# Kernel optimization log

Hardware: AMD Instinct MI355X
Metric: run time of the kernel (lower is better)

The kernel has to match this reference:

```python
import jax, jax.numpy as jnp
import numpy as np

# --- dims (match init_kwargs) ---
B, T, S, K = 4, 128, 64, 2
CS = 1024            # codebook_size
NOTE_V, PHON_V = 128, 64
NE, PE, SE, PGB, PGE = 128, 128, 16, 8, 32
COND, TOK, PREV, D = 256, 256, 256, 512
NH, L_CTX, L_AUD = 8, 4, 6
HIST_WIN, AUD_WIN = 32, 64
DFF = 4 * D

CTX_KEYS = ["ln1_w","ln1_b","in_w","in_b","out_w","out_b","ln2_w","ln2_b","f1_w","f1_b","f2_w","f2_b"]


def _ln(x, w, b):
    m = x.mean(-1, keepdims=True)
    v = ((x - m) ** 2).mean(-1, keepdims=True)
    return (x - m) / jnp.sqrt(v + 1e-5) * w + b


def _mlp2(x, w1, b1, w2, b2, act):
    return act(x @ w1.T + b1) @ w2.T + b2


def _local_mask(n, win):
    i = jnp.arange(n)
    d = i[:, None] - i[None, :]
    return (d < 0) | (d >= win)   # True = masked (causal, local window)


def _mha(x, mask, in_w, in_b, out_w, out_b, nh):
    b, s, d = x.shape
    dh = d // nh
    q, k, v = jnp.split(x @ in_w.T + in_b, 3, axis=-1)
    sp = lambda t: t.reshape(b, s, nh, dh).transpose(0, 2, 1, 3)
    q, k, v = sp(q), sp(k), sp(v)
    sc = jnp.einsum('bhqd,bhkd->bhqk', q, k) * (1.0 / np.sqrt(dh))
    sc = jnp.where(mask, -1e9, sc)
    a = jax.nn.softmax(sc, axis=-1)
    o = jnp.einsum('bhqk,bhkd->bhqd', a, v).transpose(0, 2, 1, 3).reshape(b, s, d)
    return o @ out_w.T + out_b


def _block(x, mask, pr, nh):
    # pr: dict with ln1_w..f2_b for one layer (pre-norm attn + FFN, GELU)
    h = _ln(x, pr["ln1_w"], pr["ln1_b"])
    x = x + _mha(h, mask, pr["in_w"], pr["in_b"], pr["out_w"], pr["out_b"], nh)
    h2 = _ln(x, pr["ln2_w"], pr["ln2_b"])
    return x + _mlp2(h2, pr["f1_w"], pr["f1_b"], pr["f2_w"], pr["f2_b"],
                     lambda z: jax.nn.gelu(z, approximate=False))


def _forward(p, codes, note_id, phoneme_id, slur, phone_progress):
    silu = jax.nn.silu
    # ---- condition encoder ----
    cond_in = jnp.concatenate([
        p["note_emb_w"][note_id], p["phoneme_emb_w"][phoneme_id],
        p["slur_emb_w"][jnp.clip(slur, 0, 1)], p["pp_emb_w"][phone_progress]], -1)
    cond = _mlp2(cond_in, p["cond_w1"], p["cond_b1"], p["cond_w2"], p["cond_b2"], silu)
    # ---- shifted prev-step representation ----
    first = codes[..., 0]                       # [B,T,S]
    pooled = p["token_emb_w"][first].mean(2)    # [B,T,TOK]
    prev = _mlp2(pooled, p["prev_w1"], p["prev_b1"], p["prev_w2"], p["prev_b2"], silu)
    bos = jnp.broadcast_to(p["bos_step"], (B, 1, PREV))
    prev = jnp.concatenate([bos, prev[:, :-1]], 1)
    # ---- context transformer over steps (local causal window) ----
    h = _mlp2(jnp.concatenate([cond, prev], -1), p["step_w1"], p["step_b1"], p["step_w2"], p["step_b2"], silu)
    m_ctx = _local_mask(T, HIST_WIN)
    for l in range(L_CTX):
        pr = {k: p["ctx_" + k][l] for k in CTX_KEYS}
        h = _block(h, m_ctx, pr, NH)
    # ---- audio decoder over frames within each step ----
    tok = p["token_emb_w"][first] @ p["audio_in_w"].T + p["audio_in_b"]   # [B,T,S,D]
    bos_a = jnp.broadcast_to(p["audio_bos"], (B, T, 1, D))
    a = jnp.concatenate([bos_a, tok[:, :, :-1]], 2) + p["frame_pos"][None, None] + h[:, :, None]
    a = a.reshape(B * T, S, D)
    m_a = _local_mask(S, min(AUD_WIN, S))
    for l in range(L_AUD):
        pr = {k: p["aud_" + k][l] for k in CTX_KEYS}
        a = _block(a, m_a, pr, NH)
    ah = a.reshape(B, T, S, D)
    # ---- heads ----
    first_logits = (ah @ p["first_w"].T + p["first_b"])[..., None, :]     # [B,T,S,1,CS]
    rh = _mlp2(jnp.concatenate([ah, tok], -1), p["resc_w1"], p["resc_b1"], p["resc_w2"], p["resc_b2"], silu)
    res = jnp.einsum('btsd,kcd->btskc', rh, p["res_w"]) + p["res_b"]       # [B,T,S,K-1,CS]
    return jnp.concatenate([first_logits, res], axis=3)                    # [B,T,S,K,CS]


def setup_inputs() -> dict:
    key = jax.random.key(0)
    ks = iter(jax.random.split(key, 128))
    w = lambda *sh: jax.random.normal(next(ks), sh, jnp.float32) * 0.02
    z = lambda *sh: jnp.zeros(sh, jnp.float32)
    o = lambda *sh: jnp.ones(sh, jnp.float32)
    inp = {
        "codes": jax.random.randint(next(ks), (B, T, S, K), 0, CS, jnp.int32),
        "note_id": jax.random.randint(next(ks), (B, T), 0, NOTE_V, jnp.int32),
        "phoneme_id": jax.random.randint(next(ks), (B, T), 0, PHON_V, jnp.int32),
        "slur": jax.random.randint(next(ks), (B, T), 0, 2, jnp.int32),
        "phone_progress": jax.random.randint(next(ks), (B, T), 0, PGB, jnp.int32),
        "note_emb_w": w(NOTE_V, NE), "phoneme_emb_w": w(PHON_V, PE),
        "slur_emb_w": w(2, SE), "pp_emb_w": w(PGB, PGE),
        "cond_w1": w(COND, NE + PE + SE + PGE), "cond_b1": z(COND),
        "cond_w2": w(COND, COND), "cond_b2": z(COND),
        "token_emb_w": w(CS, TOK),
        "prev_w1": w(PREV, TOK), "prev_b1": z(PREV),
        "prev_w2": w(PREV, PREV), "prev_b2": z(PREV),
        "bos_step": z(PREV),
        "step_w1": w(D, COND + PREV), "step_b1": z(D),
        "step_w2": w(D, D), "step_b2": z(D),
        "audio_in_w": w(D, TOK), "audio_in_b": z(D),
        "audio_bos": z(D), "frame_pos": w(S, D),
        "first_w": w(CS, D), "first_b": z(CS),
        "resc_w1": w(D, 2 * D), "resc_b1": z(D),
        "resc_w2": w(D, D), "resc_b2": z(D),
        "res_w": w(K - 1, CS, D), "res_b": z(K - 1, CS),
    }
    for pre, L in (("ctx_", L_CTX), ("aud_", L_AUD)):
        inp[pre + "ln1_w"] = o(L, D); inp[pre + "ln1_b"] = z(L, D)
        inp[pre + "in_w"] = w(L, 3 * D, D); inp[pre + "in_b"] = z(L, 3 * D)
        inp[pre + "out_w"] = w(L, D, D); inp[pre + "out_b"] = z(L, D)
        inp[pre + "ln2_w"] = o(L, D); inp[pre + "ln2_b"] = z(L, D)
        inp[pre + "f1_w"] = w(L, DFF, D); inp[pre + "f1_b"] = z(L, DFF)
        inp[pre + "f2_w"] = w(L, D, DFF); inp[pre + "f2_b"] = z(L, D)
    return inp


FLOAT_KEYS = ["note_emb_w","phoneme_emb_w","slur_emb_w","pp_emb_w","cond_w1","cond_b1","cond_w2","cond_b2","token_emb_w","prev_w1","prev_b1","prev_w2","prev_b2","bos_step","step_w1","step_b1","step_w2","step_b2","audio_in_w","audio_in_b","audio_bos","frame_pos","first_w","first_b","resc_w1","resc_b1","resc_w2","resc_b2","res_w","res_b"] + [p + k for p in ("ctx_","aud_") for k in CTX_KEYS]


def reference(codes, note_id, phoneme_id, slur, phone_progress,
              note_emb_w, phoneme_emb_w, slur_emb_w, pp_emb_w,
              cond_w1, cond_b1, cond_w2, cond_b2, token_emb_w,
              prev_w1, prev_b1, prev_w2, prev_b2, bos_step,
              step_w1, step_b1, step_w2, step_b2,
              audio_in_w, audio_in_b, audio_bos, frame_pos,
              first_w, first_b, resc_w1, resc_b1, resc_w2, resc_b2, res_w, res_b,
              ctx_ln1_w, ctx_ln1_b, ctx_in_w, ctx_in_b, ctx_out_w, ctx_out_b,
              ctx_ln2_w, ctx_ln2_b, ctx_f1_w, ctx_f1_b, ctx_f2_w, ctx_f2_b,
              aud_ln1_w, aud_ln1_b, aud_in_w, aud_in_b, aud_out_w, aud_out_b,
              aud_ln2_w, aud_ln2_b, aud_f1_w, aud_f1_b, aud_f2_w, aud_f2_b):
    loc = locals()
    p = {k: loc[k] for k in FLOAT_KEYS}
    return _forward(p, codes, note_id, phoneme_id, slur, phone_progress)
```

## Files before the change

kernel.cpp:

```cpp
#include <hip/hip_runtime.h>
#include <cstdint>
#include <cstddef>

typedef unsigned short u16;
typedef short bf16x8 __attribute__((ext_vector_type(8)));
typedef float f32x4 __attribute__((ext_vector_type(4)));

__device__ __forceinline__ float bf2f(u16 u) { return __uint_as_float(((unsigned)u) << 16); }
__device__ __forceinline__ u16 f2bf(float f) {
  unsigned i = __float_as_uint(f);
  i += 0x7fffu + ((i >> 16) & 1u);
  return (u16)(i >> 16);
}
__device__ __forceinline__ unsigned packbf2(float lo, float hi) {
  return (unsigned)f2bf(lo) | ((unsigned)f2bf(hi) << 16);
}
__device__ __forceinline__ float lo16(unsigned u) { return __uint_as_float(u << 16); }
__device__ __forceinline__ float hi16(unsigned u) { return __uint_as_float(u & 0xffff0000u); }

__device__ __forceinline__ void async_ld16(u16* lds, const u16* g) {
  __builtin_amdgcn_global_load_lds((const __attribute__((address_space(1))) void*)g,
                                   (__attribute__((address_space(3))) void*)lds, 16, 0, 0);
}

__global__ void k_cast8(const float4* __restrict__ x, uint4* __restrict__ y, int n8) {
  int i = blockIdx.x * 256 + threadIdx.x;
  if (i >= n8) return;
  float4 a = x[(size_t)i * 2], b = x[(size_t)i * 2 + 1];
  uint4 o;
  o.x = packbf2(a.x, a.y); o.y = packbf2(a.z, a.w);
  o.z = packbf2(b.x, b.y); o.w = packbf2(b.z, b.w);
  y[i] = o;
}

template<int ACT, int OUTM>
__global__ __launch_bounds__(256)
void gemm_mfma(const u16* __restrict__ A, const u16* __restrict__ W,
               const float* __restrict__ bias, void* __restrict__ Cp,
               int M, int N, int K, int ldc) {
  __shared__ u16 As[3][128 * 32];
  __shared__ u16 Bs[3][128 * 32];
  const int tid = threadIdx.x;
  const int wave = tid >> 6, lane = tid & 63;

  const int gx = gridDim.x;
  const int nwg = gx * (int)gridDim.y;
  const int flat = (int)blockIdx.y * gx + (int)blockIdx.x;
  const int xcd = flat & 7, lo = flat >> 3;
  const int q = nwg >> 3, r = nwg & 7;
  const int swz = (xcd < r ? xcd * (q + 1) : r * (q + 1) + (xcd - r) * q) + lo;
  const int bm = (swz / gx) * 128, bn = (swz % gx) * 128;

  const int wm = (wave & 1) * 64, wn = (wave >> 1) * 64;
  const int srow = tid >> 2, selem = (tid & 3) * 8;
  const u16* Ap0 = A + (size_t)(bm + srow) * K + selem;
  const u16* Ap1 = A + (size_t)(bm + srow + 64) * K + selem;
  const u16* Wp0 = W + (size_t)(bn + srow) * K + selem;
  const u16* Wp1 = W + (size_t)(bn + srow + 64) * K + selem;
  const int fr = lane & 15, fq = (lane >> 4) * 8;

  f32x4 acc[4][4];
#pragma unroll
  for (int i = 0; i < 4; ++i)
#pragma unroll
    for (int j = 0; j < 4; ++j) acc[i][j] = (f32x4){0.f, 0.f, 0.f, 0.f};

  const int nt = K >> 5;

  auto stage = [&](int buf, int k0) {
    u16* AsD = &As[buf][tid * 8];
    u16* BsD = &Bs[buf][tid * 8];
    async_ld16(AsD, Ap0 + k0);
    async_ld16(AsD + 2048, Ap1 + k0);
    async_ld16(BsD, Wp0 + k0);
    async_ld16(BsD + 2048, Wp1 + k0);
  };

  stage(0, 0);
  if (nt > 1) stage(1, 32);

  int bi = 0;
  for (int t = 0; t < nt; ++t) {
    if (t + 1 < nt) asm volatile("s_waitcnt vmcnt(4)" ::: "memory");
    else            asm volatile("s_waitcnt vmcnt(0)" ::: "memory");
    __builtin_amdgcn_s_barrier();
    if (t + 2 < nt) {
      int nb = bi + 2; if (nb >= 3) nb -= 3;
      stage(nb, (t + 2) << 5);
    }
    const u16* Asb = As[bi];
    const u16* Bsb = Bs[bi];
    bf16x8 af[4], bfv[4];
#pragma unroll
    for (int i = 0; i < 4; ++i)
      af[i] = *(const bf16x8*)&Asb[(wm + i * 16 + fr) * 32 + fq];
#pragma unroll
    for (int j = 0; j < 4; ++j)
      bfv[j] = *(const bf16x8*)&Bsb[(wn + j * 16 + fr) * 32 + fq];
#pragma unroll
    for (int i = 0; i < 4; ++i)
#pragma unroll
      for (int j = 0; j < 4; ++j)
        acc[i][j] = __builtin_amdgcn_mfma_f32_16x16x32_bf16(af[i], bfv[j], acc[i][j], 0, 0, 0);
    if (++bi == 3) bi = 0;
  }

  const int mr = bm + wm + (lane >> 4) * 4;
  const int nc = bn + wn + (lane & 15);
#pragma unroll
  for (int j = 0; j < 4; ++j) {
    int n = nc + j * 16;
    float bv = bias[n];
#pragma unroll
    for (int i = 0; i < 4; ++i) {
      int mbase = mr + i * 16;
#pragma unroll
      for (int r = 0; r < 4; ++r) {
        float v = acc[i][j][r] + bv;
        if (ACT == 1) v = v / (1.f + __expf(-v));
        else if (ACT == 2) v = 0.5f * v * (1.f + erff(v * 0.70710678118f));
        size_t off = (size_t)(mbase + r) * ldc + n;
        if (OUTM == 0) ((u16*)Cp)[off] = f2bf(v);
        else if (OUTM == 1) ((float*)Cp)[off] += v;
        else ((float*)Cp)[off] = v;
      }
    }
  }
}

__global__ __launch_bounds__(256)
void k_layernorm(const float* __restrict__ X, const float* __restrict__ w,
                 const float* __restrict__ b, u16* __restrict__ Y) {
  int row = blockIdx.x, tid = threadIdx.x;
  const float* x = X + (size_t)row * 512;
  float v0 = x[tid], v1 = x[tid + 256];
  __shared__ float red[4];
  float s = v0 + v1;
  for (int o = 32; o; o >>= 1) s += __shfl_down(s, o, 64);
  if ((tid & 63) == 0) red[tid >> 6] = s;
  __syncthreads();
  if (tid == 0) red[0] = (red[0] + red[1] + red[2] + red[3]) * (1.f / 512.f);
  __syncthreads();
  float mean = red[0];
  __syncthreads();
  float d0 = v0 - mean, d1 = v1 - mean;
  float q = d0 * d0 + d1 * d1;
  for (int o = 32; o; o >>= 1) q += __shfl_down(q, o, 64);
  if ((tid & 63) == 0) red[tid >> 6] = q;
  __syncthreads();
  if (tid == 0) red[0] = (red[0] + red[1] + red[2] + red[3]) * (1.f / 512.f);
  __syncthreads();
  float rstd = rsqrtf(red[0] + 1e-5f);
  size_t o0 = (size_t)row * 512 + tid;
  Y[o0] = f2bf(d0 * rstd * w[tid] + b[tid]);
  Y[o0 + 256] = f2bf(d1 * rstd * w[tid + 256] + b[tid + 256]);
}

__global__ void k_cond_gather(const int* __restrict__ note_id, const int* __restrict__ phon_id,
                              const int* __restrict__ slur, const int* __restrict__ pp,
                              const float* __restrict__ note_emb, const float* __restrict__ phon_emb,
                              const float* __restrict__ slur_emb, const float* __restrict__ pp_emb,
                              u16* __restrict__ out) {
  int bt = blockIdx.x, t = threadIdx.x;
  u16 v = 0;
  if (t < 128) v = f2bf(note_emb[note_id[bt] * 128 + t]);
  else if (t < 256) v = f2bf(phon_emb[phon_id[bt] * 128 + (t - 128)]);
  else if (t < 272) {
    int sv = slur[bt]; sv = sv < 0 ? 0 : (sv > 1 ? 1 : sv);
    v = f2bf(slur_emb[sv * 16 + (t - 256)]);
  } else if (t < 304) v = f2bf(pp_emb[pp[bt] * 32 + (t - 272)]);
  out[bt * 320 + t] = v;
}

__global__ void k_pad_w(const float* __restrict__ w, u16* __restrict__ out) {
  int n = blockIdx.x, t = threadIdx.x;
  out[n * 320 + t] = (t < 304) ? f2bf(w[n * 304 + t]) : (u16)0;
}

__global__ void k_femb(const int* __restrict__ codes, const uint4* __restrict__ emb,
                       uint4* __restrict__ out) {
  int i = blockIdx.x * 256 + threadIdx.x;
  int m = i >> 5, c = i & 31;
  out[i] = emb[(size_t)codes[m * 2] * 32 + c];
}

__global__ void k_pool(const u16* __restrict__ femb, u16* __restrict__ pooled) {
  int bt = blockIdx.x, c = threadIdx.x;
  float s = 0.f;
  for (int j = 0; j < 64; ++j) s += bf2f(femb[((size_t)bt * 64 + j) * 256 + c]);
  pooled[bt * 256 + c] = f2bf(s * (1.f / 64.f));
}

__global__ void k_stepin(const u16* __restrict__ cond, const u16* __restrict__ prevo,
                         const float* __restrict__ bosf, u16* __restrict__ out) {
  int bt = blockIdx.x, t = threadIdx.x;
  u16 v;
  if (t < 256) v = cond[bt * 256 + t];
  else {
    int tt = bt & 127;
    v = (tt == 0) ? f2bf(bosf[t - 256]) : prevo[(bt - 1) * 256 + (t - 256)];
  }
  out[bt * 512 + t] = v;
}

__global__ __launch_bounds__(64)
void k_ctx_attn(const u16* __restrict__ qkv, u16* __restrict__ out) {
  int t = blockIdx.x, h = blockIdx.y, b = blockIdx.z;
  int lane = threadIdx.x;
  int bt = b * 128 + t;
  float qd = bf2f(qkv[(size_t)bt * 1536 + h * 64 + lane]) * 0.125f;
  int klo = t - 31; if (klo < 0) klo = 0;
  int n = t - klo + 1;
  __shared__ float sc[32];
  for (int i = 0; i < n; ++i) {
    float p = qd * bf2f(qkv[((size_t)(b * 128 + klo + i)) * 1536 + 512 + h * 64 + lane]);
    for (int o = 32; o; o >>= 1) p += __shfl_xor(p, o, 64);
    if (lane == 0) sc[i] = p;
  }
  __syncthreads();
  float mx = -1e30f;
  for (int i = 0; i < n; ++i) mx = fmaxf(mx, sc[i]);
  float den = 0.f, acc = 0.f;
  for (int i = 0; i < n; ++i) {
    float p = __expf(sc[i] - mx);
    den += p;
    acc += p * bf2f(qkv[((size_t)(b * 128 + klo + i)) * 1536 + 1024 + h * 64 + lane]);
  }
  out[(size_t)bt * 512 + h * 64 + lane] = f2bf(acc / den);
}

__global__ __launch_bounds__(128)
void k_aud_attn_mfma(const u16* __restrict__ qkv, u16* __restrict__ out) {
  constexpr int LP = 66;
  __shared__ u16 Pl[2][64 * LP];
  __shared__ u16 Vt[2][64 * LP];
  const int wave = threadIdx.x >> 6, lane = threadIdx.x & 63;
  const int id = blockIdx.x * 2 + wave;
  const int seq = id >> 3, h = id & 7;
  const u16* Qb = qkv + (size_t)seq * 64 * 1536 + h * 64;
  const u16* Kb = Qb + 512;
  const u16* Vb = Qb + 1024;
  u16* Plw = Pl[wave];
  u16* Vtw = Vt[wave];
  const int fr = lane & 15, fq = (lane >> 4) * 8;

#pragma unroll
  for (int t = 0; t < 8; ++t) {
    int vr = (lane >> 3) + 8 * t, vc = (lane & 7) * 8;
    uint4 vv = *(const uint4*)(Vb + (size_t)vr * 1536 + vc);
    Vtw[(vc + 0) * LP + vr] = (u16)(vv.x & 0xffff);
    Vtw[(vc + 1) * LP + vr] = (u16)(vv.x >> 16);
    Vtw[(vc + 2) * LP + vr] = (u16)(vv.y & 0xffff);
    Vtw[(vc + 3) * LP + vr] = (u16)(vv.y >> 16);
    Vtw[(vc + 4) * LP + vr] = (u16)(vv.z & 0xffff);
    Vtw[(vc + 5) * LP + vr] = (u16)(vv.z >> 16);
    Vtw[(vc + 6) * LP + vr] = (u16)(vv.w & 0xffff);
    Vtw[(vc + 7) * LP + vr] = (u16)(vv.w >> 16);
  }

  bf16x8 aq[4][2], bk[4][2];
#pragma unroll
  for (int i = 0; i < 4; ++i)
#pragma unroll
    for (int c = 0; c < 2; ++c) {
      aq[i][c] = *(const bf16x8*)(Qb + (size_t)(i * 16 + fr) * 1536 + fq + 32 * c);
      bk[i][c] = *(const bf16x8*)(Kb + (size_t)(i * 16 + fr) * 1536 + fq + 32 * c);
    }
  f32x4 s[4][4];
#pragma unroll
  for (int i = 0; i < 4; ++i)
#pragma unroll
    for (int j = 0; j < 4; ++j) s[i][j] = (f32x4){0.f, 0.f, 0.f, 0.f};
#pragma unroll
  for (int c = 0; c < 2; ++c)
#pragma unroll
    for (int i = 0; i < 4; ++i)
#pragma unroll
      for (int j = 0; j < 4; ++j)
        s[i][j] = __builtin_amdgcn_mfma_f32_16x16x32_bf16(aq[i][c], bk[j][c], s[i][j], 0, 0, 0);

  const int qr = (lane >> 4) * 4;
#pragma unroll
  for (int i = 0; i < 4; ++i) {
#pragma unroll
    for (int r = 0; r < 4; ++r) {
      int row = 16 * i + qr + r;
      float mx = -1e30f;
      float vj[4];
#pragma unroll
      for (int j = 0; j < 4; ++j) {
        float v = s[i][j][r] * 0.125f;
        if (16 * j + fr > row) v = -1e30f;
        vj[j] = v;
        mx = fmaxf(mx, v);
      }
      for (int o = 8; o; o >>= 1) mx = fmaxf(mx, __shfl_xor(mx, o, 64));
      float den = 0.f;
#pragma unroll
      for (int j = 0; j < 4; ++j) { vj[j] = __expf(vj[j] - mx); den += vj[j]; }
      for (int o = 8; o; o >>= 1) den += __shfl_xor(den, o, 64);
      float inv = 1.f / den;
#pragma unroll
      for (int j = 0; j < 4; ++j)
        Plw[row * LP + 16 * j + fr] = f2bf(vj[j] * inv);
    }
  }
  __syncthreads();

  f32x4 o4[4][4];
#pragma unroll
  for (int i = 0; i < 4; ++i)
#pragma unroll
    for (int j = 0; j < 4; ++j) o4[i][j] = (f32x4){0.f, 0.f, 0.f, 0.f};
#pragma unroll
  for (int c = 0; c < 2; ++c) {
    bf16x8 ap[4], bv[4];
#pragma unroll
    for (int i = 0; i < 4; ++i)
      ap[i] = *(const bf16x8*)&Plw[(16 * i + fr) * LP + fq + 32 * c];
#pragma unroll
    for (int j = 0; j < 4; ++j)
      bv[j] = *(const bf16x8*)&Vtw[(16 * j + fr) * LP + fq + 32 * c];
#pragma unroll
    for (int i = 0; i < 4; ++i)
#pragma unroll
      for (int j = 0; j < 4; ++j)
        o4[i][j] = __builtin_amdgcn_mfma_f32_16x16x32_bf16(ap[i], bv[j], o4[i][j], 0, 0, 0);
  }
#pragma unroll
  for (int i = 0; i < 4; ++i)
#pragma unroll
    for (int r = 0; r < 4; ++r) {
      int row = 16 * i + qr + r;
      u16* ob = out + ((size_t)seq * 64 + row) * 512 + h * 64;
#pragma unroll
      for (int j = 0; j < 4; ++j) ob[16 * j + fr] = f2bf(o4[i][j][r]);
    }
}

__global__ void k_abuild(const uint4* __restrict__ tok, const float4* __restrict__ bosf,
                         const float4* __restrict__ fpos, const float4* __restrict__ hstep,
                         float4* __restrict__ a) {
  size_t i = (size_t)blockIdx.x * 256 + threadIdx.x;
  int d8 = (int)(i & 63);
  size_t row = i >> 6;
  int s = (int)(row & 63);
  size_t bt = row >> 6;
  float t0, t1, t2, t3, t4, t5, t6, t7;
  if (s == 0) {
    float4 b0 = bosf[d8 * 2], b1 = bosf[d8 * 2 + 1];
    t0 = b0.x; t1 = b0.y; t2 = b0.z; t3 = b0.w;
    t4 = b1.x; t5 = b1.y; t6 = b1.z; t7 = b1.w;
  } else {
    uint4 tv = tok[(row - 1) * 64 + d8];
    t0 = lo16(tv.x); t1 = hi16(tv.x); t2 = lo16(tv.y); t3 = hi16(tv.y);
    t4 = lo16(tv.z); t5 = hi16(tv.z); t6 = lo16(tv.w); t7 = hi16(tv.w);
  }
  float4 f0 = fpos[(size_t)s * 128 + d8 * 2], f1 = fpos[(size_t)s * 128 + d8 * 2 + 1];
  float4 h0 = hstep[bt * 128 + d8 * 2], h1 = hstep[bt * 128 + d8 * 2 + 1];
  float4 o0, o1;
  o0.x = t0 + f0.x + h0.x; o0.y = t1 + f0.y + h0.y;
  o0.z = t2 + f0.z + h0.z; o0.w = t3 + f0.w + h0.w;
  o1.x = t4 + f1.x + h1.x; o1.y = t5 + f1.y + h1.y;
  o1.z = t6 + f1.z + h1.z; o1.w = t7 + f1.w + h1.w;
  a[i * 2] = o0; a[i * 2 + 1] = o1;
}

__global__ void k_cat(const uint4* __restrict__ ah, const uint4* __restrict__ tok,
                      uint4* __restrict__ out) {
  size_t i = (size_t)blockIdx.x * 256 + threadIdx.x;
  size_t m = i >> 7;
  int c = (int)(i & 127);
  out[i] = (c < 64) ? ah[m * 64 + c] : tok[m * 64 + (c - 64)];
}

template<int ACT, int OUTM>
static inline void gemm(const u16* A, const u16* W, const float* bias, void* C,
                        int M, int N, int K, int ldc, hipStream_t s) {
  gemm_mfma<ACT, OUTM><<<dim3(N / 128, M / 128), 256, 0, s>>>(A, W, bias, C, M, N, K, ldc);
}

static inline void cast_bf16(const float* x, u16* y, size_t n, hipStream_t s) {
  int n8 = (int)(n / 8);
  k_cast8<<<(n8 + 255) / 256, 256, 0, s>>>((const float4*)x, (uint4*)y, n8);
}

extern "C" void kernel_launch(void* const* d_in, const int* in_sizes, int n_in,
                              void* d_out, int out_size, void* d_ws, size_t ws_size,
                              hipStream_t stream) {
  const int* codes    = (const int*)d_in[0];
  const int* note_id  = (const int*)d_in[1];
  const int* phon_id  = (const int*)d_in[2];
  const int* slur     = (const int*)d_in[3];
  const int* pprog    = (const int*)d_in[4];
  const float* note_emb = (const float*)d_in[5];
  const float* phon_emb = (const float*)d_in[6];
  const float* slur_emb = (const float*)d_in[7];
  const float* pp_emb   = (const float*)d_in[8];
  const float* cond_w1  = (const float*)d_in[9];
  const float* cond_b1  = (const float*)d_in[10];
  const float* cond_w2  = (const float*)d_in[11];
  const float* cond_b2  = (const float*)d_in[12];
  const float* tok_emb  = (const float*)d_in[13];
  const float* prev_w1  = (const float*)d_in[14];
  const float* prev_b1  = (const float*)d_in[15];
  const float* prev_w2  = (const float*)d_in[16];
  const float* prev_b2  = (const float*)d_in[17];
  const float* bos_step = (const float*)d_in[18];
  const float* step_w1  = (const float*)d_in[19];
  const float* step_b1  = (const float*)d_in[20];
  const float* step_w2  = (const float*)d_in[21];
  const float* step_b2  = (const float*)d_in[22];
  const float* audio_in_w = (const float*)d_in[23];
  const float* audio_in_b = (const float*)d_in[24];
  const float* audio_bos  = (const float*)d_in[25];
  const float* frame_pos  = (const float*)d_in[26];
  const float* first_w  = (const float*)d_in[27];
  const float* first_b  = (const float*)d_in[28];
  const float* resc_w1  = (const float*)d_in[29];
  const float* resc_b1  = (const float*)d_in[30];
  const float* resc_w2  = (const float*)d_in[31];
  const float* resc_b2  = (const float*)d_in[32];
  const float* res_w    = (const float*)d_in[33];
  const float* res_b    = (const float*)d_in[34];
  const float* ctx_w[12]; for (int i = 0; i < 12; ++i) ctx_w[i] = (const float*)d_in[35 + i];
  const float* aud_w[12]; for (int i = 0; i < 12; ++i) aud_w[i] = (const float*)d_in[47 + i];

  char* p = (char*)d_ws;
  auto alloc = [&](size_t b) { char* r = p; p += (b + 255) & ~(size_t)255; return r; };
  float* A_res = (float*)alloc(32768ull * 512 * 4);
  u16* T_tok  = (u16*)alloc(32768ull * 512 * 2);
  u16* LNb    = (u16*)alloc(32768ull * 512 * 2);
  u16* AOb    = (u16*)alloc(32768ull * 512 * 2);
  u16* QF     = (u16*)alloc(32768ull * 2048 * 2);
  u16* f_emb  = (u16*)alloc(32768ull * 256 * 2);
  u16* temb   = (u16*)alloc(1024ull * 256 * 2);
  u16* cond_in = (u16*)alloc(512ull * 320 * 2);
  u16* cw1p   = (u16*)alloc(256ull * 320 * 2);
  u16* cw2    = (u16*)alloc(256ull * 256 * 2);
  u16* pw1    = (u16*)alloc(256ull * 256 * 2);
  u16* pw2    = (u16*)alloc(256ull * 256 * 2);
  u16* sw1    = (u16*)alloc(512ull * 512 * 2);
  u16* sw2    = (u16*)alloc(512ull * 512 * 2);
  u16* ainw   = (u16*)alloc(512ull * 256 * 2);
  u16* fw     = (u16*)alloc(1024ull * 512 * 2);
  u16* rw1    = (u16*)alloc(512ull * 1024 * 2);
  u16* rw2    = (u16*)alloc(512ull * 512 * 2);
  u16* resw   = (u16*)alloc(1024ull * 512 * 2);
  u16* cxin   = (u16*)alloc(4ull * 1536 * 512 * 2);
  u16* cxout  = (u16*)alloc(4ull * 512 * 512 * 2);
  u16* cxf1   = (u16*)alloc(4ull * 2048 * 512 * 2);
  u16* cxf2   = (u16*)alloc(4ull * 512 * 2048 * 2);
  u16* adin   = (u16*)alloc(6ull * 1536 * 512 * 2);
  u16* adout  = (u16*)alloc(6ull * 512 * 512 * 2);
  u16* adf1   = (u16*)alloc(6ull * 2048 * 512 * 2);
  u16* adf2   = (u16*)alloc(6ull * 512 * 2048 * 2);
  u16* cond_h = (u16*)alloc(512ull * 256 * 2);
  u16* condv  = (u16*)alloc(512ull * 256 * 2);
  u16* pooled = (u16*)alloc(512ull * 256 * 2);
  u16* prevh  = (u16*)alloc(512ull * 256 * 2);
  u16* prevo  = (u16*)alloc(512ull * 256 * 2);
  u16* stepin = (u16*)alloc(512ull * 512 * 2);
  u16* hmid   = (u16*)alloc(512ull * 512 * 2);
  float* hstep = (float*)alloc(512ull * 512 * 4);

  k_pad_w<<<256, 320, 0, stream>>>(cond_w1, cw1p);
  cast_bf16(cond_w2, cw2, 256ull * 256, stream);
  cast_bf16(prev_w1, pw1, 256ull * 256, stream);
  cast_bf16(prev_w2, pw2, 256ull * 256, stream);
  cast_bf16(step_w1, sw1, 512ull * 512, stream);
  cast_bf16(step_w2, sw2, 512ull * 512, stream);
  cast_bf16(tok_emb, temb, 1024ull * 256, stream);
  cast_bf16(audio_in_w, ainw, 512ull * 256, stream);
  cast_bf16(first_w, fw, 1024ull * 512, stream);
  cast_bf16(resc_w1, rw1, 512ull * 1024, stream);
  cast_bf16(resc_w2, rw2, 512ull * 512, stream);
  cast_bf16(res_w, resw, 1024ull * 512, stream);
  cast_bf16(ctx_w[2], cxin, 4ull * 1536 * 512, stream);
  cast_bf16(ctx_w[4], cxout, 4ull * 512 * 512, stream);
  cast_bf16(ctx_w[8], cxf1, 4ull * 2048 * 512, stream);
  cast_bf16(ctx_w[10], cxf2, 4ull * 512 * 2048, stream);
  cast_bf16(aud_w[2], adin, 6ull * 1536 * 512, stream);
  cast_bf16(aud_w[4], adout, 6ull * 512 * 512, stream);
  cast_bf16(aud_w[8], adf1, 6ull * 2048 * 512, stream);
  cast_bf16(aud_w[10], adf2, 6ull * 512 * 2048, stream);

  k_cond_gather<<<512, 320, 0, stream>>>(note_id, phon_id, slur, pprog,
                                         note_emb, phon_emb, slur_emb, pp_emb, cond_in);
  k_femb<<<4096, 256, 0, stream>>>(codes, (const uint4*)temb, (uint4*)f_emb);
  k_pool<<<512, 256, 0, stream>>>(f_emb, pooled);
  gemm<1, 0>(cond_in, cw1p, cond_b1, cond_h, 512, 256, 320, 256, stream);
  gemm<0, 0>(cond_h, cw2, cond_b2, condv, 512, 256, 256, 256, stream);
  gemm<1, 0>(pooled, pw1, prev_b1, prevh, 512, 256, 256, 256, stream);
  gemm<0, 0>(prevh, pw2, prev_b2, prevo, 512, 256, 256, 256, stream);
  k_stepin<<<512, 512, 0, stream>>>(condv, prevo, bos_step, stepin);
  gemm<1, 0>(stepin, sw1, step_b1, hmid, 512, 512, 512, 512, stream);
  gemm<0, 2>(hmid, sw2, step_b2, hstep, 512, 512, 512, 512, stream);

  for (int l = 0; l < 4; ++l) {
    k_layernorm<<<512, 256, 0, stream>>>(hstep, ctx_w[0] + l * 512, ctx_w[1] + l * 512, LNb);
    gemm<0, 0>(LNb, cxin + (size_t)l * 1536 * 512, ctx_w[3] + l * 1536, QF, 512, 1536, 512, 1536, stream);
    k_ctx_attn<<<dim3(128, 8, 4), 64, 0, stream>>>(QF, AOb);
    gemm<0, 1>(AOb, cxout + (size_t)l * 512 * 512, ctx_w[5] + l * 512, hstep, 512, 512, 512, 512, stream);
    k_layernorm<<<512, 256, 0, stream>>>(hstep, ctx_w[6] + l * 512, ctx_w[7] + l * 512, LNb);
    gemm<2, 0>(LNb, cxf1 + (size_t)l * 2048 * 512, ctx_w[9] + l * 2048, QF, 512, 2048, 512, 2048, stream);
    gemm<0, 1>(QF, cxf2 + (size_t)l * 512 * 2048, ctx_w[11] + l * 512, hstep, 512, 512, 2048, 512, stream);
  }

  gemm<0, 0>(f_emb, ainw, audio_in_b, T_tok, 32768, 512, 256, 512, stream);
  k_abuild<<<8192, 256, 0, stream>>>((const uint4*)T_tok, (const float4*)audio_bos,
                                     (const float4*)frame_pos, (const float4*)hstep, (float4*)A_res);
  for (int l = 0; l < 6; ++l) {
    k_layernorm<<<32768, 256, 0, stream>>>(A_res, aud_w[0] + l * 512, aud_w[1] + l * 512, LNb);
    gemm<0, 0>(LNb, adin + (size_t)l * 1536 * 512, aud_w[3] + l * 1536, QF, 32768, 1536, 512, 1536, stream);
    k_aud_attn_mfma<<<2048, 128, 0, stream>>>(QF, AOb);
    gemm<0, 1>(AOb, adout + (size_t)l * 512 * 512, aud_w[5] + l * 512, A_res, 32768, 512, 512, 512, stream);
    k_layernorm<<<32768, 256, 0, stream>>>(A_res, aud_w[6] + l * 512, aud_w[7] + l * 512, LNb);
    gemm<2, 0>(LNb, adf1 + (size_t)l * 2048 * 512, aud_w[9] + l * 2048, QF, 32768, 2048, 512, 2048, stream);
    gemm<0, 1>(QF, adf2 + (size_t)l * 512 * 2048, aud_w[11] + l * 512, A_res, 32768, 512, 2048, 512, stream);
  }

  {
    int n8 = 32768 * 512 / 8;
    k_cast8<<<(n8 + 255) / 256, 256, 0, stream>>>((const float4*)A_res, (uint4*)LNb, n8);
  }
  gemm<0, 2>(LNb, fw, first_b, (float*)d_out, 32768, 1024, 512, 2048, stream);
  k_cat<<<16384, 256, 0, stream>>>((const uint4*)LNb, (const uint4*)T_tok, (uint4*)QF);
  gemm<1, 0>(QF, rw1, resc_b1, AOb, 32768, 512, 1024, 512, stream);
  gemm<0, 0>(AOb, rw2, resc_b2, T_tok, 32768, 512, 512, 512, stream);
  gemm<0, 2>(T_tok, resw, res_b, (float*)d_out + 1024, 32768, 1024, 512, 2048, stream);
}
```

Measured before the change: 4.280 ms.

## Add 256x256-tile MFMA GEMM with 4-stage async pipeline for audio-stage matmuls

Adds a second GEMM kernel that uses 256x256 output tiles, 512 threads (8 waves), a four-buffer async global-to-LDS pipeline with explicit vmcnt waits, and an XCD-aware block swizzle. All the large M=32768 GEMMs in the audio transformer and output heads now use it, while the small context GEMMs keep the 128x128 kernel. The goal is more data reuse per LDS load and better latency hiding on the dominant GEMMs. In exchange it needs about 128KB of LDS per block, which limits occupancy to one block per CU, and it raises register pressure from 32 accumulator tiles per wave.

```diff
diff --git a/kernel.cpp b/kernel.cpp
--- a/kernel.cpp
+++ b/kernel.cpp
@@ -120,6 +120,112 @@
         if (ACT == 1) v = v / (1.f + __expf(-v));
         else if (ACT == 2) v = 0.5f * v * (1.f + erff(v * 0.70710678118f));
         size_t off = (size_t)(mbase + r) * ldc + n;
+        if (OUTM == 0) ((u16*)Cp)[off] = f2bf(v);
+        else if (OUTM == 1) ((float*)Cp)[off] += v;
+        else ((float*)Cp)[off] = v;
+      }
+    }
+  }
+}
+
+template<int ACT, int OUTM>
+__global__ __launch_bounds__(512, 2)
+void gemm_mfma256(const u16* __restrict__ A, const u16* __restrict__ W,
+                  const float* __restrict__ bias, void* __restrict__ Cp,
+                  int M, int N, int K, int ldc) {
+  __shared__ u16 As[4][256 * 32];
+  __shared__ u16 Bs[4][256 * 32];
+  const int tid = threadIdx.x;
+  const int wave = tid >> 6, lane = tid & 63;
+  const int wave_m = wave >> 2, wave_n = wave & 3;
+  const int WM = wave_m * 128, WN = wave_n * 64;
+
+  const int gx = gridDim.x;
+  const int nwg = gx * (int)gridDim.y;
+  const int flat = (int)blockIdx.y * gx + (int)blockIdx.x;
+  const int xcd = flat & 7, lo = flat >> 3;
+  const int q = nwg >> 3, r = nwg & 7;
+  const int swz = (xcd < r ? xcd * (q + 1) : r * (q + 1) + (xcd - r) * q) + lo;
+  const int bm = (swz / gx) * 256, bn = (swz % gx) * 256;
+
+  const int srow = tid >> 2;
+  const int sl = ((tid & 3) ^ ((tid >> 3) & 3)) * 8;
+  const u16* Ap0 = A + (size_t)(bm + srow) * K + sl;
+  const u16* Ap1 = A + (size_t)(bm + 128 + srow) * K + sl;
+  const u16* Wp0 = W + (size_t)(bn + srow) * K + sl;
+  const u16* Wp1 = W + (size_t)(bn + 128 + srow) * K + sl;
+
+  const int fr = lane & 15;
+  const int pA = (((lane >> 4) ^ ((fr >> 1) & 3))) * 8;
+  const int aoff = (WM + fr) * 32 + pA;
+  const int boff = (WN + fr) * 32 + pA;
+
+  f32x4 acc[8][4];
+#pragma unroll
+  for (int i = 0; i < 8; ++i)
+#pragma unroll
+    for (int j = 0; j < 4; ++j) acc[i][j] = (f32x4){0.f, 0.f, 0.f, 0.f};
+
+  const int nt = K >> 5;
+
+  auto stage = [&](int buf, int k0) {
+    u16* AsD = &As[buf][tid * 8];
+    u16* BsD = &Bs[buf][tid * 8];
+    async_ld16(AsD, Ap0 + k0);
+    async_ld16(AsD + 4096, Ap1 + k0);
+    async_ld16(BsD, Wp0 + k0);
+    async_ld16(BsD + 4096, Wp1 + k0);
+  };
+
+#pragma unroll 1
+  for (int s = 0; s < 4 && s < nt; ++s) stage(s, s << 5);
+
+#pragma unroll 1
+  for (int t = 0; t < nt; ++t) {
+    int infl = (t == 0) ? 3 : 2;
+    int rem = nt - 1 - t; if (infl > rem) infl = rem;
+    if (infl >= 3)      asm volatile("s_waitcnt vmcnt(12)" ::: "memory");
+    else if (infl == 2) asm volatile("s_waitcnt vmcnt(8)" ::: "memory");
+    else if (infl == 1) asm volatile("s_waitcnt vmcnt(4)" ::: "memory");
+    else                asm volatile("s_waitcnt vmcnt(0)" ::: "memory");
+    __builtin_amdgcn_sched_barrier(0);
+    __builtin_amdgcn_s_barrier();
+    __builtin_amdgcn_sched_barrier(0);
+    if (t >= 1 && t + 3 < nt) stage((t + 3) & 3, (t + 3) << 5);
+
+    const u16* Asb = As[t & 3];
+    const u16* Bsb = Bs[t & 3];
+    bf16x8 af[8], bfv[4];
+#pragma unroll
+    for (int i = 0; i < 8; ++i)
+      af[i] = *(const bf16x8*)&Asb[aoff + i * 512];
+#pragma unroll
+    for (int j = 0; j < 4; ++j)
+      bfv[j] = *(const bf16x8*)&Bsb[boff + j * 512];
+    __builtin_amdgcn_s_setprio(1);
+#pragma unroll
+    for (int i = 0; i < 8; ++i)
+#pragma unroll
+      for (int j = 0; j < 4; ++j)
+        acc[i][j] = __builtin_amdgcn_mfma_f32_16x16x32_bf16(af[i], bfv[j], acc[i][j], 0, 0, 0);
+    __builtin_amdgcn_s_setprio(0);
+  }
+
+  const int mr = bm + WM + (lane >> 4) * 4;
+  const int nc = bn + WN + fr;
+#pragma unroll
+  for (int j = 0; j < 4; ++j) {
+    int n = nc + j * 16;
+    float bv = bias[n];
+#pragma unroll
+    for (int i = 0; i < 8; ++i) {
+      int mbase = mr + i * 16;
+#pragma unroll
+      for (int rr = 0; rr < 4; ++rr) {
+        float v = acc[i][j][rr] + bv;
+        if (ACT == 1) v = v / (1.f + __expf(-v));
+        else if (ACT == 2) v = 0.5f * v * (1.f + erff(v * 0.70710678118f));
+        size_t off = (size_t)(mbase + rr) * ldc + n;
         if (OUTM == 0) ((u16*)Cp)[off] = f2bf(v);
         else if (OUTM == 1) ((float*)Cp)[off] += v;
         else ((float*)Cp)[off] = v;
@@ -378,6 +484,12 @@
 static inline void gemm(const u16* A, const u16* W, const float* bias, void* C,
                         int M, int N, int K, int ldc, hipStream_t s) {
   gemm_mfma<ACT, OUTM><<<dim3(N / 128, M / 128), 256, 0, s>>>(A, W, bias, C, M, N, K, ldc);
+}
+
+template<int ACT, int OUTM>
+static inline void gemmBig(const u16* A, const u16* W, const float* bias, void* C,
+                           int M, int N, int K, int ldc, hipStream_t s) {
+  gemm_mfma256<ACT, OUTM><<<dim3(N / 256, M / 256), 512, 0, s>>>(A, W, bias, C, M, N, K, ldc);
 }
 
 static inline void cast_bf16(const float* x, u16* y, size_t n, hipStream_t s) {
@@ -507,26 +619,26 @@
     gemm<0, 1>(QF, cxf2 + (size_t)l * 512 * 2048, ctx_w[11] + l * 512, hstep, 512, 512, 2048, 512, stream);
   }
 
-  gemm<0, 0>(f_emb, ainw, audio_in_b, T_tok, 32768, 512, 256, 512, stream);
+  gemmBig<0, 0>(f_emb, ainw, audio_in_b, T_tok, 32768, 512, 256, 512, stream);
   k_abuild<<<8192, 256, 0, stream>>>((const uint4*)T_tok, (const float4*)audio_bos,
                                      (const float4*)frame_pos, (const float4*)hstep, (float4*)A_res);
   for (int l = 0; l < 6; ++l) {
     k_layernorm<<<32768, 256, 0, stream>>>(A_res, aud_w[0] + l * 512, aud_w[1] + l * 512, LNb);
-    gemm<0, 0>(LNb, adin + (size_t)l * 1536 * 512, aud_w[3] + l * 1536, QF, 32768, 1536, 512, 1536, stream);
+    gemmBig<0, 0>(LNb, adin + (size_t)l * 1536 * 512, aud_w[3] + l * 1536, QF, 32768, 1536, 512, 1536, stream);
     k_aud_attn_mfma<<<2048, 128, 0, stream>>>(QF, AOb);
-    gemm<0, 1>(AOb, adout + (size_t)l * 512 * 512, aud_w[5] + l * 512, A_res, 32768, 512, 512, 512, stream);
+    gemmBig<0, 1>(AOb, adout + (size_t)l * 512 * 512, aud_w[5] + l * 512, A_res, 32768, 512, 512, 512, stream);
     k_layernorm<<<32768, 256, 0, stream>>>(A_res, aud_w[6] + l * 512, aud_w[7] + l * 512, LNb);
-    gemm<2, 0>(LNb, adf1 + (size_t)l * 2048 * 512, aud_w[9] + l * 2048, QF, 32768, 2048, 512, 2048, stream);
-    gemm<0, 1>(QF, adf2 + (size_t)l * 512 * 2048, aud_w[11] + l * 512, A_res, 32768, 512, 2048, 512, stream);
+    gemmBig<2, 0>(LNb, adf1 + (size_t)l * 2048 * 512, aud_w[9] + l * 2048, QF, 32768, 2048, 512, 2048, stream);
+    gemmBig<0, 1>(QF, adf2 + (size_t)l * 512 * 2048, aud_w[11] + l * 512, A_res, 32768, 512, 2048, 512, stream);
   }
 
   {
     int n8 = 32768 * 512 / 8;
     k_cast8<<<(n8 + 255) / 256, 256, 0, stream>>>((const float4*)A_res, (uint4*)LNb, n8);
   }
-  gemm<0, 2>(LNb, fw, first_b, (float*)d_out, 32768, 1024, 512, 2048, stream);
+  gemmBig<0, 2>(LNb, fw, first_b, (float*)d_out, 32768, 1024, 512, 2048, stream);
   k_cat<<<16384, 256, 0, stream>>>((const uint4*)LNb, (const uint4*)T_tok, (uint4*)QF);
-  gemm<1, 0>(QF, rw1, resc_b1, AOb, 32768, 512, 1024, 512, stream);
-  gemm<0, 0>(AOb, rw2, resc_b2, T_tok, 32768, 512, 512, 512, stream);
-  gemm<0, 2>(T_tok, resw, res_b, (float*)d_out + 1024, 32768, 1024, 512, 2048, stream);
-}
+  gemmBig<1, 0>(QF, rw1, resc_b1, AOb, 32768, 512, 1024, 512, stream);
+  gemmBig<0, 0>(AOb, rw2, resc_b2, T_tok, 32768, 512, 512, 512, stream);
+  gemmBig<0, 2>(T_tok, resw, res_b, (float*)d_out + 1024, 32768, 1024, 512, 2048, stream);
+}
```

After: 4.811 ms. 1.12x slower.
